# Kernel optimization log

Measured on AMD Instinct MI355X. Metric: run time of the kernel, lower is better.

## Reference

```python
import jax, jax.numpy as jnp
import numpy as np

B, S = 32, 32
G_RATIO = 0.5
H_W = 1.0
N_STEPS = int(0.95 * S * S)  # training-mode Tmax
SQRT_SIZE = float(np.sqrt(S))
SQRT2 = float(np.sqrt(2.0))

_NF = np.ones((3, 3), np.float32); _NF[1, 1] = 0.0                      # 8-neighbor filter
_CF = np.ones((3, 3), np.float32); _CF[1, 1] = 0.0
_CF[0, 0] = _CF[0, 2] = _CF[2, 0] = _CF[2, 2] = SQRT2                   # diagonal move cost


def conv3x3(x, filt):
    # x: [B,S,S], filt: [3,3] -> SAME conv (matches F.conv2d(padding=1) with one shared filter)
    return jax.lax.conv_general_dilated(x[:, None], filt[None, None], (1, 1), 'SAME')[:, 0]


def diag_heuristic(goal):
    # goal: [B,S,S] one-hot
    ii, jj = jnp.meshgrid(jnp.arange(S), jnp.arange(S), indexing='ij')
    loc = jnp.stack([ii, jj], 0).astype(goal.dtype)                     # [2,S,S]
    goal_loc = jnp.einsum('kij,bij->bk', loc, goal)                     # [B,2]
    dxdy = jnp.abs(loc.reshape(2, -1)[None] - goal_loc[:, :, None])     # [B,2,S*S]
    h = dxdy.min(axis=1) * SQRT2 + jnp.abs(dxdy[:, 0] - dxdy[:, 1])
    return h.reshape(goal.shape)


def astar_core(start, goal, obst):
    nf = jnp.asarray(_NF)
    cf = jnp.asarray(_CF)
    h = diag_heuristic(goal) * H_W
    g0 = jnp.zeros_like(start)
    hist0 = jnp.zeros_like(start)
    goal_idx = jnp.argmax(goal.reshape(B, -1), axis=-1)                 # goal one-hot index
    parents0 = jnp.ones((B, S * S), start.dtype) * goal_idx[:, None].astype(start.dtype)

    def step(carry, _):
        g, open_m, hist, parents, done = carry
        f = G_RATIO * g + (1.0 - G_RATIO + 0.001) * h
        f_exp = jnp.exp(-f / SQRT_SIZE) * open_m
        # straight-through softmax-argmax selection
        v = f_exp.reshape(B, -1)
        y = v / v.sum(-1, keepdims=True)
        ind = jnp.argmax(y, axis=-1)                                    # [B]
        y_hard = jax.nn.one_hot(ind, S * S, dtype=y.dtype)
        sel = (jax.lax.stop_gradient(y_hard - y) + y).reshape(B, S, S)
        dist = (sel * goal).sum((1, 2), keepdims=True)
        unsolved = (dist < 1e-8).astype(f.dtype)
        hist_n = jnp.clip(hist + sel, 0.0, 1.0)
        open_n = jnp.clip(open_m - unsolved * sel, 0.0, 1.0)
        nbr = conv3x3(sel, nf) * obst
        g2 = (g * sel).sum((1, 2), keepdims=True) + conv3x3(sel, cf)
        idx = jax.lax.stop_gradient(
            ((1.0 - open_n) * (1.0 - hist_n) + open_n * (g > g2).astype(f.dtype)) * nbr)
        g_n = jax.lax.stop_gradient(g2 * idx + g * (1.0 - idx))
        open_n = jax.lax.stop_gradient(jnp.clip(open_n + idx, 0.0, 1.0))
        idxf = idx.reshape(B, -1)
        parents_n = ind[:, None].astype(parents.dtype) * idxf + parents * (1.0 - idxf)
        keep = lambda old, new: jnp.where(done, old, new)               # freeze after break point
        carry_n = (keep(g, g_n), keep(open_m, open_n), keep(hist, hist_n),
                   keep(parents, parents_n), done | jnp.all(unsolved == 0))
        return carry_n, None

    init = (g0, start, hist0, parents0, jnp.array(False))
    (g, open_m, hist, parents, done), _ = jax.lax.scan(step, init, None, length=N_STEPS)

    # backtrack (idempotent past the true path length, so run fixed N_STEPS iters)
    pi = jax.lax.stop_gradient(parents).astype(jnp.int32)
    gl = goal.reshape(B, -1).astype(jnp.int32)
    rows = jnp.arange(B)
    loc0 = (pi * gl).sum(-1)

    def bt(i, st):
        path, loc = st
        path = path.at[rows, loc].set(1)
        return path, pi[rows, loc]

    path, _ = jax.lax.fori_loop(0, N_STEPS, bt, (gl, loc0))
    return hist, path.reshape(B, S, S), g


def setup_inputs() -> dict:
    key = jax.random.key(0)
    k1, k2, k3, k4 = jax.random.split(key, 4)
    rows = jnp.arange(B)
    start_idx = jax.random.randint(k2, (B,), 0, S * S // 2)
    goal_idx = jax.random.randint(k3, (B,), S * S // 2, S * S)
    obst = (jax.random.uniform(k1, (B, S, S)) > 0.15).astype(jnp.float32)
    # guarantee start->goal connectivity: clear start's column and goal's row
    obst = obst.at[rows, :, start_idx % S].set(1.0)
    obst = obst.at[rows, goal_idx // S, :].set(1.0)
    start = jax.nn.one_hot(start_idx, S * S, dtype=jnp.float32).reshape(B, 1, S, S)
    goal = jax.nn.one_hot(goal_idx, S * S, dtype=jnp.float32).reshape(B, 1, S, S)
    cost = jax.random.normal(k4, (B, 1, S, S), dtype=jnp.float32)  # unused in 'default' mode
    return {"cost_maps": cost, "start_maps": start, "goal_maps": goal,
            "obstacles_maps": obst[:, None]}


def reference(cost_maps, start_maps, goal_maps, obstacles_maps):
    # mode='default': cost_maps is replaced by zeros in the torch code (unused)
    hist, path, g = astar_core(start_maps[:, 0], goal_maps[:, 0], obstacles_maps[:, 0])
    return hist[:, None], path[:, None], g[:, None]
```

## Files before the change

### kernel.cpp

```cpp
#include <hip/hip_runtime.h>

#define BATCH 32
#define SS 1024
#define NSTEPS 972
#define LSTR 20

#define UNVIS   0x7F000000u
#define CLOSEDB 0x7F000001u
#define OBSTB   0x7F000002u

typedef unsigned long long ull;

template <int CTRL>
__device__ __forceinline__ int dpp32(int v) {
    return __builtin_amdgcn_update_dpp(v, v, CTRL, 0xF, 0xF, false);
}

__device__ __forceinline__ float wave_min_f32_bcast(float v) {
    float t;
    t = __int_as_float(dpp32<0xB1 >(__float_as_int(v))); v = fminf(v, t);
    t = __int_as_float(dpp32<0x4E >(__float_as_int(v))); v = fminf(v, t);
    t = __int_as_float(dpp32<0x141>(__float_as_int(v))); v = fminf(v, t);
    t = __int_as_float(dpp32<0x140>(__float_as_int(v))); v = fminf(v, t);
    t = __int_as_float(dpp32<0x142>(__float_as_int(v))); v = fminf(v, t);
    t = __int_as_float(dpp32<0x143>(__float_as_int(v))); v = fminf(v, t);
    return __int_as_float(__builtin_amdgcn_readlane(__float_as_int(v), 63));
}

__device__ __forceinline__ float grp8_min_f32(float v) {
    float t;
    t = __int_as_float(dpp32<0xB1 >(__float_as_int(v))); v = fminf(v, t);
    t = __int_as_float(dpp32<0x4E >(__float_as_int(v))); v = fminf(v, t);
    t = __int_as_float(dpp32<0x141>(__float_as_int(v))); v = fminf(v, t);
    return v;
}

__device__ __forceinline__ unsigned umin2(unsigned a, unsigned b) { return a < b ? a : b; }
__device__ __forceinline__ float fmin3(float a, float b, float c) { return fminf(fminf(a, b), c); }
__device__ __forceinline__ unsigned umin3(unsigned a, unsigned b, unsigned c) { return umin2(umin2(a, b), c); }
__device__ __forceinline__ unsigned slotc(float v, unsigned lm, unsigned i) {
    return (__float_as_uint(v) == lm) ? i : 63u;
}

__global__ __launch_bounds__(64)
void astar_kernel(const float* __restrict__ start_maps,
                  const float* __restrict__ goal_maps,
                  const float* __restrict__ obst_maps,
                  float* __restrict__ out)
{
    const int b = blockIdx.x;
    const int lane = threadIdx.x;

    __shared__ __align__(16) float fop[64 * LSTR];
    __shared__ __align__(16) float g_s[SS];
    __shared__ unsigned short par_s[SS];
    __shared__ int sh_start, sh_goal;

    const float* st = start_maps + b * SS;
    const float* gl = goal_maps + b * SS;
    const float* ob = obst_maps + b * SS;

    for (int i = 0; i < 16; ++i) {
        int c = i * 64 + lane;
        if (st[c] > 0.5f) sh_start = c;
        if (gl[c] > 0.5f) sh_goal = c;
    }
    __syncthreads();
    const int start_idx = sh_start;
    const int goal_idx = sh_goal;
    const float gi = (float)(goal_idx >> 5);
    const float gj = (float)(goal_idx & 31);
    const float SQRT2F = 1.41421356237309515f;
    const float WH = 0.501f;
    const float INFF = __int_as_float(0x7f800000);
    const float CB = __uint_as_float(CLOSEDB);

    for (int i = 0; i < 16; ++i) {
        int c = i * 64 + lane;
        g_s[c] = 0.0f;
        par_s[c] = (unsigned short)goal_idx;
        fop[(c >> 4) * LSTR + (c & 15)] = __uint_as_float(ob[c] > 0.5f ? UNVIS : OBSTB);
    }
    __syncthreads();
    if (lane == 0) {
        float dx0 = fabsf((float)(start_idx >> 5) - gi);
        float dy0 = fabsf((float)(start_idx & 31) - gj);
        float h0 = __fadd_rn(__fmul_rn(fminf(dx0, dy0), SQRT2F), fabsf(dx0 - dy0));
        fop[(start_idx >> 4) * LSTR + (start_idx & 15)] = __fmul_rn(WH, h0);
    }
    __syncthreads();

    const float* frow = &fop[lane * LSTR];
    int sel = start_idx;

    #pragma unroll 1
    for (int step = 0; step < NSTEPS; ++step) {
        const bool solved = (sel == goal_idx);
        const int si = sel >> 5, sj = sel & 31;

        if (lane == 0)
            fop[(sel >> 4) * LSTR + (sel & 15)] = CB;
        asm volatile("" ::: "memory");

        float4 r0 = *(const float4*)(frow + 0);
        float4 r1 = *(const float4*)(frow + 4);
        float4 r2 = *(const float4*)(frow + 8);
        float4 r3 = *(const float4*)(frow + 12);
        asm volatile("" ::: "memory");

        int k8 = lane < 8 ? (lane < 4 ? lane : lane + 1) : 4;
        int di = k8 / 3 - 1;
        int dj = k8 - (k8 / 3) * 3 - 1;
        int ni = si + di, nj = sj + dj;
        bool act = (lane < 8) && ((unsigned)ni < 32u) && ((unsigned)nj < 32u);
        int nb = act ? ni * 32 + nj : sel;
        int fa = (nb >> 4) * LSTR + (nb & 15);
        unsigned fbv = __float_as_uint(fop[fa]);
        float gnb = g_s[nb];
        float gsel = g_s[sel];

        float a0 = fminf(fmin3(r0.x, r0.y, r0.z), r0.w);
        float a1 = fminf(fmin3(r1.x, r1.y, r1.z), r1.w);
        float a2 = fminf(fmin3(r2.x, r2.y, r2.z), r2.w);
        float a3 = fminf(fmin3(r3.x, r3.y, r3.z), r3.w);
        float lmin = fminf(fmin3(a0, a1, a2), a3);
        const unsigned lm = __float_as_uint(lmin);
        const float gs = wave_min_f32_bcast(lmin);

        unsigned s0 = umin3(umin3(slotc(r0.x, lm, 0),  slotc(r0.y, lm, 1),  slotc(r0.z, lm, 2)),
                            umin3(slotc(r0.w, lm, 3),  slotc(r1.x, lm, 4),  slotc(r1.y, lm, 5)),
                            umin2(slotc(r1.z, lm, 6),  slotc(r1.w, lm, 7)));
        unsigned s1 = umin3(umin3(slotc(r2.x, lm, 8),  slotc(r2.y, lm, 9),  slotc(r2.z, lm, 10)),
                            umin3(slotc(r2.w, lm, 11), slotc(r3.x, lm, 12), slotc(r3.y, lm, 13)),
                            umin2(slotc(r3.z, lm, 14), slotc(r3.w, lm, 15)));
        unsigned slot = umin2(s0, s1);

        float dxn = fabsf((float)ni - gi);
        float dyn = fabsf((float)nj - gj);
        float hn  = __fadd_rn(__fmul_rn(fminf(dxn, dyn), SQRT2F), fabsf(dxn - dyn));
        float fhn = __fmul_rn(WH, hn);

        float w = ((di != 0) && (dj != 0)) ? SQRT2F : 1.0f;
        float g2 = __fadd_rn(gsel, w);
        bool rel = act && ((fbv == UNVIS) || (fbv < UNVIS && gnb > g2));
        float fnew = __fadd_rn(__fmul_rn(0.5f, g2), fhn);
        if (rel) {
            fop[fa] = fnew;
            g_s[nb] = g2;
            par_s[nb] = (unsigned short)sel;
        }
        if (solved) break;

        float fv = rel ? fnew : INFF;
        float fm = grp8_min_f32(fv);
        const float fmv = __int_as_float(__builtin_amdgcn_readlane(__float_as_int(fm), 0));

        const float gmin = fminf(gs, fmv);
        const unsigned gb = __float_as_uint(gmin);
        const ull bal_s = __ballot(lm == gb);
        const ull bal_f = __ballot(__float_as_uint(fv) == gb);

        unsigned idx_s = 0xFFFFu, idx_f = 0xFFFFu;
        if (bal_s) {
            int owner = (int)__builtin_ctzll(bal_s);
            idx_s = (unsigned)(owner * 16 + __builtin_amdgcn_readlane((int)slot, owner));
        }
        if (bal_f) {
            int fl = (int)__builtin_ctzll(bal_f);
            idx_f = (unsigned)__builtin_amdgcn_readlane(nb, fl);
        }
        sel = (int)umin2(idx_s, idx_f);
    }

    float* out_hist = out + b * SS;
    float* out_path = out + BATCH * SS + b * SS;
    float* out_g    = out + 2 * BATCH * SS + b * SS;
    for (int i = 0; i < 16; ++i) {
        int c = i * 64 + lane;
        unsigned fbv = __float_as_uint(fop[(c >> 4) * LSTR + (c & 15)]);
        out_hist[c] = (fbv == CLOSEDB) ? 1.0f : 0.0f;
        out_g[c]    = g_s[c];
        out_path[c] = (c == goal_idx) ? 1.0f : 0.0f;
    }
    __syncthreads();
    if (lane == 0) {
        int loc = par_s[goal_idx];
        for (int it = 0; it < NSTEPS; ++it) {
            out_path[loc] = 1.0f;
            if (loc == goal_idx) break;
            loc = par_s[loc];
        }
    }
}

extern "C" void kernel_launch(void* const* d_in, const int* in_sizes, int n_in,
                              void* d_out, int out_size, void* d_ws, size_t ws_size,
                              hipStream_t stream)
{
    const float* start_maps = (const float*)d_in[1];
    const float* goal_maps  = (const float*)d_in[2];
    const float* obst_maps  = (const float*)d_in[3];
    float* out = (float*)d_out;
    hipLaunchKernelGGL(astar_kernel, dim3(BATCH), dim3(64), 0, stream,
                       start_maps, goal_maps, obst_maps, out);
}
```

Before: 41.19 us.

## Software-pipeline per-step LDS row loads and patch the closed cell in registers

Each lane's 16-entry row of f values is now loaded right after the relax writes of the current step, and carried into the next step in registers. The load is issued before the neighbor-min reduction and ballot/readlane selection, so its LDS latency can overlap that work instead of sitting at the top of the loop. The node closed at the start of a step is patched into the register copy by comparison, so the min still sees it as closed. The loop is manually unrolled by two with double-buffered float4 registers, and the initial start f write is dropped because the first selection is fixed to the start anyway. The trade-off is more register pressure and extra select instructions per step.

```diff
diff --git a/kernel.cpp b/kernel.cpp
--- a/kernel.cpp
+++ b/kernel.cpp
@@ -36,10 +36,13 @@
 }
 
 __device__ __forceinline__ unsigned umin2(unsigned a, unsigned b) { return a < b ? a : b; }
-__device__ __forceinline__ float fmin3(float a, float b, float c) { return fminf(fminf(a, b), c); }
-__device__ __forceinline__ unsigned umin3(unsigned a, unsigned b, unsigned c) { return umin2(umin2(a, b), c); }
 __device__ __forceinline__ unsigned slotc(float v, unsigned lm, unsigned i) {
     return (__float_as_uint(v) == lm) ? i : 63u;
+}
+
+template <int S>
+__device__ __forceinline__ float patchf(float K, unsigned csel) {
+    return (csel == (unsigned)S) ? __uint_as_float(CLOSEDB) : K;
 }
 
 __global__ __launch_bounds__(64)
@@ -82,30 +85,25 @@
         fop[(c >> 4) * LSTR + (c & 15)] = __uint_as_float(ob[c] > 0.5f ? UNVIS : OBSTB);
     }
     __syncthreads();
-    if (lane == 0) {
-        float dx0 = fabsf((float)(start_idx >> 5) - gi);
-        float dy0 = fabsf((float)(start_idx & 31) - gj);
-        float h0 = __fadd_rn(__fmul_rn(fminf(dx0, dy0), SQRT2F), fabsf(dx0 - dy0));
-        fop[(start_idx >> 4) * LSTR + (start_idx & 15)] = __fmul_rn(WH, h0);
-    }
-    __syncthreads();
 
     const float* frow = &fop[lane * LSTR];
+    float4 A0 = *(const float4*)(frow + 0);
+    float4 A1 = *(const float4*)(frow + 4);
+    float4 A2 = *(const float4*)(frow + 8);
+    float4 A3 = *(const float4*)(frow + 12);
+    float4 B0 = A0, B1 = A1, B2 = A2, B3 = A3;
+
     int sel = start_idx;
-
-    #pragma unroll 1
-    for (int step = 0; step < NSTEPS; ++step) {
-        const bool solved = (sel == goal_idx);
+    bool solved = false;
+
+    auto STEP = [&](float4& t0, float4& t1, float4& t2, float4& t3,
+                    float4& l0, float4& l1, float4& l2, float4& l3)
+    {
+        solved = (sel == goal_idx);
         const int si = sel >> 5, sj = sel & 31;
 
         if (lane == 0)
             fop[(sel >> 4) * LSTR + (sel & 15)] = CB;
-        asm volatile("" ::: "memory");
-
-        float4 r0 = *(const float4*)(frow + 0);
-        float4 r1 = *(const float4*)(frow + 4);
-        float4 r2 = *(const float4*)(frow + 8);
-        float4 r3 = *(const float4*)(frow + 12);
         asm volatile("" ::: "memory");
 
         int k8 = lane < 8 ? (lane < 4 ? lane : lane + 1) : 4;
@@ -119,27 +117,37 @@
         float gnb = g_s[nb];
         float gsel = g_s[sel];
 
-        float a0 = fminf(fmin3(r0.x, r0.y, r0.z), r0.w);
-        float a1 = fminf(fmin3(r1.x, r1.y, r1.z), r1.w);
-        float a2 = fminf(fmin3(r2.x, r2.y, r2.z), r2.w);
-        float a3 = fminf(fmin3(r3.x, r3.y, r3.z), r3.w);
-        float lmin = fminf(fmin3(a0, a1, a2), a3);
+        const unsigned csel = (lane == (sel >> 4)) ? (unsigned)(sel & 15) : 64u;
+        float q00 = patchf<0 >(t0.x, csel), q01 = patchf<1 >(t0.y, csel);
+        float q02 = patchf<2 >(t0.z, csel), q03 = patchf<3 >(t0.w, csel);
+        float q04 = patchf<4 >(t1.x, csel), q05 = patchf<5 >(t1.y, csel);
+        float q06 = patchf<6 >(t1.z, csel), q07 = patchf<7 >(t1.w, csel);
+        float q08 = patchf<8 >(t2.x, csel), q09 = patchf<9 >(t2.y, csel);
+        float q10 = patchf<10>(t2.z, csel), q11 = patchf<11>(t2.w, csel);
+        float q12 = patchf<12>(t3.x, csel), q13 = patchf<13>(t3.y, csel);
+        float q14 = patchf<14>(t3.z, csel), q15 = patchf<15>(t3.w, csel);
+        float a0 = fminf(fminf(q00, q01), fminf(q02, q03));
+        float a1 = fminf(fminf(q04, q05), fminf(q06, q07));
+        float a2 = fminf(fminf(q08, q09), fminf(q10, q11));
+        float a3 = fminf(fminf(q12, q13), fminf(q14, q15));
+        float lmin = fminf(fminf(a0, a1), fminf(a2, a3));
         const unsigned lm = __float_as_uint(lmin);
         const float gs = wave_min_f32_bcast(lmin);
 
-        unsigned s0 = umin3(umin3(slotc(r0.x, lm, 0),  slotc(r0.y, lm, 1),  slotc(r0.z, lm, 2)),
-                            umin3(slotc(r0.w, lm, 3),  slotc(r1.x, lm, 4),  slotc(r1.y, lm, 5)),
-                            umin2(slotc(r1.z, lm, 6),  slotc(r1.w, lm, 7)));
-        unsigned s1 = umin3(umin3(slotc(r2.x, lm, 8),  slotc(r2.y, lm, 9),  slotc(r2.z, lm, 10)),
-                            umin3(slotc(r2.w, lm, 11), slotc(r3.x, lm, 12), slotc(r3.y, lm, 13)),
-                            umin2(slotc(r3.z, lm, 14), slotc(r3.w, lm, 15)));
-        unsigned slot = umin2(s0, s1);
+        unsigned s0 = umin2(umin2(slotc(q00, lm, 0),  slotc(q01, lm, 1)),
+                            umin2(slotc(q02, lm, 2),  slotc(q03, lm, 3)));
+        unsigned s1 = umin2(umin2(slotc(q04, lm, 4),  slotc(q05, lm, 5)),
+                            umin2(slotc(q06, lm, 6),  slotc(q07, lm, 7)));
+        unsigned s2 = umin2(umin2(slotc(q08, lm, 8),  slotc(q09, lm, 9)),
+                            umin2(slotc(q10, lm, 10), slotc(q11, lm, 11)));
+        unsigned s3 = umin2(umin2(slotc(q12, lm, 12), slotc(q13, lm, 13)),
+                            umin2(slotc(q14, lm, 14), slotc(q15, lm, 15)));
+        unsigned slot = umin2(umin2(s0, s1), umin2(s2, s3));
 
         float dxn = fabsf((float)ni - gi);
         float dyn = fabsf((float)nj - gj);
         float hn  = __fadd_rn(__fmul_rn(fminf(dxn, dyn), SQRT2F), fabsf(dxn - dyn));
         float fhn = __fmul_rn(WH, hn);
-
         float w = ((di != 0) && (dj != 0)) ? SQRT2F : 1.0f;
         float g2 = __fadd_rn(gsel, w);
         bool rel = act && ((fbv == UNVIS) || (fbv < UNVIS && gnb > g2));
@@ -149,7 +157,13 @@
             g_s[nb] = g2;
             par_s[nb] = (unsigned short)sel;
         }
-        if (solved) break;
+        asm volatile("" ::: "memory");
+
+        l0 = *(const float4*)(frow + 0);
+        l1 = *(const float4*)(frow + 4);
+        l2 = *(const float4*)(frow + 8);
+        l3 = *(const float4*)(frow + 12);
+        asm volatile("" ::: "memory");
 
         float fv = rel ? fnew : INFF;
         float fm = grp8_min_f32(fv);
@@ -170,6 +184,14 @@
             idx_f = (unsigned)__builtin_amdgcn_readlane(nb, fl);
         }
         sel = (int)umin2(idx_s, idx_f);
+    };
+
+    #pragma unroll 1
+    for (int t = 0; t < NSTEPS; t += 2) {
+        STEP(A0, A1, A2, A3, B0, B1, B2, B3);
+        if (solved) break;
+        STEP(B0, B1, B2, B3, A0, A1, A2, A3);
+        if (solved) break;
     }
 
     float* out_hist = out + b * SS;
```

Measured after the change: 43.47 us. 1.06x slower.
